# Kernel optimization log

Measured on AMD Instinct MI355X. Metric: run time of the kernel, lower is better.

## Reference

```python
import jax, jax.numpy as jnp
import numpy as np
import math

N = 20000      # nodes
E = 640000     # edges (avg degree 32)
G = 128        # g_dim (input features)
H1 = 128       # rgcn output dim
H2 = 128       # transformer output dim
R = 8          # num_relations


def setup_inputs() -> dict:
    key = jax.random.key(0)
    ks = jax.random.split(key, 12)
    x = jax.random.normal(ks[0], (N, G), dtype=jnp.float32)
    edge_index = jax.random.randint(ks[1], (2, E), 0, N)
    edge_type = jax.random.randint(ks[2], (E,), 0, R)
    s_in = 1.0 / math.sqrt(G)
    s_h1 = 1.0 / math.sqrt(H1)
    return {
        'x': x,
        'edge_index': edge_index,
        'edge_type': edge_type,
        # RGCNConv params (per-relation weights + root weight + bias)
        'rgcn_weight': jax.random.normal(ks[3], (R, G, H1), dtype=jnp.float32) * s_in,
        'rgcn_root': jax.random.normal(ks[4], (G, H1), dtype=jnp.float32) * s_in,
        'rgcn_bias': jnp.zeros((H1,), dtype=jnp.float32),
        # TransformerConv params (heads=1): query/key/value + skip linear
        'Wq': jax.random.normal(ks[5], (H1, H2), dtype=jnp.float32) * s_h1,
        'bq': jnp.zeros((H2,), dtype=jnp.float32),
        'Wk': jax.random.normal(ks[6], (H1, H2), dtype=jnp.float32) * s_h1,
        'bk': jnp.zeros((H2,), dtype=jnp.float32),
        'Wv': jax.random.normal(ks[7], (H1, H2), dtype=jnp.float32) * s_h1,
        'bv': jnp.zeros((H2,), dtype=jnp.float32),
        'Ws': jax.random.normal(ks[8], (H1, H2), dtype=jnp.float32) * s_h1,
        'bs': jnp.zeros((H2,), dtype=jnp.float32),
    }


def reference(x, edge_index, edge_type, rgcn_weight, rgcn_root, rgcn_bias,
              Wq, bq, Wk, bk, Wv, bv, Ws, bs):
    n = x.shape[0]
    src, dst = edge_index[0], edge_index[1]

    # ---- RGCNConv (aggr='mean' per relation, root weight + bias) ----
    # transform nodes by every relation, then gather per-edge message
    xr = jnp.einsum('ni,rio->nro', x, rgcn_weight)          # [N, R, H1]
    msg = xr[src, edge_type]                                # [E, H1]
    # per (dst, relation) edge counts for mean aggregation
    cnt = jnp.zeros((n, rgcn_weight.shape[0]), x.dtype).at[dst, edge_type].add(1.0)
    denom = jnp.maximum(cnt[dst, edge_type], 1.0)[:, None]  # [E, 1]
    agg = jnp.zeros((n, rgcn_weight.shape[2]), x.dtype).at[dst].add(msg / denom)
    h = agg + x @ rgcn_root + rgcn_bias
    h = jax.nn.relu(h)

    # ---- TransformerConv (heads=1, concat, root_weight=True) ----
    d = Wq.shape[1]
    q = h @ Wq + bq                                          # [N, H2]
    k = h @ Wk + bk
    v = h @ Wv + bv
    score = jnp.sum(q[dst] * k[src], axis=-1) / math.sqrt(d) # [E]
    # softmax over incoming edges of each destination node
    smax = jax.ops.segment_max(score, dst, num_segments=n)   # [N]
    e = jnp.exp(score - smax[dst])                           # [E]
    den = jax.ops.segment_sum(e, dst, num_segments=n)        # [N]
    alpha = e / jnp.maximum(den[dst], 1e-16)                 # [E]
    out = jax.ops.segment_sum(alpha[:, None] * v[src], dst, num_segments=n)
    out = out + h @ Ws + bs                                  # skip connection
    return jax.nn.relu(out)
```

## Files before the change

### kernel.cpp

```cpp
#include <hip/hip_runtime.h>

typedef unsigned short u16;
typedef unsigned int u32;
typedef __attribute__((ext_vector_type(8))) short short8;
typedef __attribute__((ext_vector_type(4))) float f32x4;

#define NN 20000
#define EE 640000
#define SCAN_BLOCKS 80

__device__ inline u16 f2bf(float f) {
    u32 x = __float_as_uint(f);
    return (u16)((x + 0x7FFFu + ((x >> 16) & 1u)) >> 16);
}
__device__ inline float lo16(u32 w) { return __uint_as_float(w << 16); }
__device__ inline float hi16(u32 w) { return __uint_as_float(w & 0xFFFF0000u); }
__device__ inline u32 packbf(float a, float b) { return ((u32)f2bf(b) << 16) | (u32)f2bf(a); }

#define ZP_N (NN * 8)
#define CX_N (NN * 32)
#define WP_N (128 * 1152 + 4 * 128 * 128 + 512)
__global__ __launch_bounds__(256) void prep_all(const float* __restrict__ x,
                                                const float* rw, const float* root,
                                                const float* Wq, const float* Wk,
                                                const float* Wv, const float* Ws,
                                                const float* bq, const float* bk,
                                                const float* bv, const float* bs,
                                                int* __restrict__ cnt, u16* __restrict__ xb,
                                                u16* wt1, u16* wt2, float* bcat) {
    int idx = blockIdx.x * 256 + threadIdx.x;
    if (idx < ZP_N) {
        cnt[idx] = 0;
        return;
    }
    idx -= ZP_N;
    if (idx < CX_N) {
        float4 v = *(const float4*)(x + (size_t)idx * 4);
        uint2 o;
        o.x = packbf(v.x, v.y);
        o.y = packbf(v.z, v.w);
        *(uint2*)(xb + (size_t)idx * 4) = o;
        return;
    }
    idx -= CX_N;
    const int S1 = 128 * 1152, S2 = 4 * 128 * 128;
    if (idx < S1) {
        int o = idx / 1152, k = idx - o * 1152;
        float v = (k < 1024) ? rw[k * 128 + o] : root[(k - 1024) * 128 + o];
        wt1[idx] = f2bf(v);
    } else if (idx < S1 + S2) {
        int j = idx - S1;
        int y = j >> 14, rem = j & 16383, o = rem >> 7, i = rem & 127;
        const float* W = (y == 0) ? Wq : (y == 1) ? Wk : (y == 2) ? Wv : Ws;
        wt2[j] = f2bf(W[i * 128 + o]);
    } else if (idx < S1 + S2 + 512) {
        int j = idx - (S1 + S2);
        int y = j >> 7, c = j & 127;
        const float* b = (y == 0) ? bq : (y == 1) ? bk : (y == 2) ? bv : bs;
        bcat[j] = b[c];
    }
}

__global__ void count_rank(const int* __restrict__ ei, const int* __restrict__ et,
                           int* __restrict__ cnt, int* __restrict__ rank) {
    int e = blockIdx.x * 256 + threadIdx.x;
    if (e >= EE) return;
    int dst = ei[EE + e];
    int r = et[e];
    rank[e] = atomicAdd(&cnt[dst * 8 + r], 1);
}

__global__ __launch_bounds__(256) void scan_phase1(const int* __restrict__ cnt,
                                                   int* __restrict__ deg_pref,
                                                   int* __restrict__ blk_sums) {
    __shared__ int lds[256];
    int t = threadIdx.x;
    int n = blockIdx.x * 256 + t;
    int d = 0;
    if (n < NN) {
        int4 c0 = *(const int4*)(cnt + n * 8);
        int4 c1 = *(const int4*)(cnt + n * 8 + 4);
        d = c0.x + c0.y + c0.z + c0.w + c1.x + c1.y + c1.z + c1.w;
    }
    lds[t] = d;
    __syncthreads();
    for (int o = 1; o < 256; o <<= 1) {
        int v = (t >= o) ? lds[t - o] : 0;
        __syncthreads();
        lds[t] += v;
        __syncthreads();
    }
    if (n < NN) deg_pref[n] = lds[t];
    if (t == 255) blk_sums[blockIdx.x] = lds[255];
}

__global__ void scan_phase2(int* __restrict__ blk_sums) {
    __shared__ int lds[128];
    int t = threadIdx.x;
    int v = (t < SCAN_BLOCKS) ? blk_sums[t] : 0;
    lds[t] = v;
    __syncthreads();
    for (int o = 1; o < 128; o <<= 1) {
        int a = (t >= o) ? lds[t - o] : 0;
        __syncthreads();
        lds[t] += a;
        __syncthreads();
    }
    if (t < SCAN_BLOCKS) blk_sums[t] = lds[t] - v;
}

__global__ __launch_bounds__(256) void scan_phase3(const int* __restrict__ cnt,
                                                   const int* __restrict__ deg_pref,
                                                   const int* __restrict__ blk_sums,
                                                   int* __restrict__ row_off,
                                                   int* __restrict__ srt) {
    int n = blockIdx.x * 256 + threadIdx.x;
    if (n >= NN) return;
    int4 c0 = *(const int4*)(cnt + n * 8);
    int4 c1 = *(const int4*)(cnt + n * 8 + 4);
    int deg = c0.x + c0.y + c0.z + c0.w + c1.x + c1.y + c1.z + c1.w;
    int start = blk_sums[blockIdx.x] + deg_pref[n] - deg;
    row_off[n] = start;
    int sub = start;
    int o[8];
    o[0] = sub; sub += c0.x;
    o[1] = sub; sub += c0.y;
    o[2] = sub; sub += c0.z;
    o[3] = sub; sub += c0.w;
    o[4] = sub; sub += c1.x;
    o[5] = sub; sub += c1.y;
    o[6] = sub; sub += c1.z;
    o[7] = sub; sub += c1.w;
    *(int4*)(srt + n * 8) = make_int4(o[0], o[1], o[2], o[3]);
    *(int4*)(srt + n * 8 + 4) = make_int4(o[4], o[5], o[6], o[7]);
    if (n == NN - 1) row_off[NN] = sub;
}

__global__ void scatter_kernel(const int* __restrict__ ei, const int* __restrict__ et,
                               const int* __restrict__ srt, const int* __restrict__ rank,
                               int* __restrict__ es) {
    int e = blockIdx.x * 256 + threadIdx.x;
    if (e >= EE) return;
    int dst = ei[EE + e];
    int src = ei[e];
    int r = et[e];
    int pos = srt[dst * 8 + r] + rank[e];
    es[pos] = src;
}

__global__ __launch_bounds__(256) void rgcn_agg(const u16* __restrict__ xb,
                                                const int* __restrict__ srt,
                                                const int* __restrict__ cnt,
                                                const int* __restrict__ es,
                                                u16* __restrict__ pre) {
    int gid = blockIdx.x * 16 + (threadIdx.x >> 4);
    int lane = threadIdx.x & 15;
    if (gid >= NN * 9) return;
    int node = gid / 9;
    int slot = gid - node * 9;
    long prebase = (long)node * 1152;
    if (slot == 8) {
        uint4 xv = *(const uint4*)(xb + (long)node * 128 + lane * 8);
        *(uint4*)(pre + prebase + 1024 + lane * 8) = xv;
        return;
    }
    int c = cnt[node * 8 + slot];
    int p0 = srt[node * 8 + slot];
    float inv = 1.0f / (float)(c > 1 ? c : 1);
    float a0 = 0.f, a1 = 0.f, a2 = 0.f, a3 = 0.f, a4 = 0.f, a5 = 0.f, a6 = 0.f, a7 = 0.f;
    int i = 0;
    for (; i + 4 <= c; i += 4) {
        int s0 = es[p0 + i], s1 = es[p0 + i + 1], s2 = es[p0 + i + 2], s3 = es[p0 + i + 3];
        uint4 w0 = *(const uint4*)(xb + (long)s0 * 128 + lane * 8);
        uint4 w1 = *(const uint4*)(xb + (long)s1 * 128 + lane * 8);
        uint4 w2 = *(const uint4*)(xb + (long)s2 * 128 + lane * 8);
        uint4 w3 = *(const uint4*)(xb + (long)s3 * 128 + lane * 8);
        a0 += (lo16(w0.x) + lo16(w1.x)) + (lo16(w2.x) + lo16(w3.x));
        a1 += (hi16(w0.x) + hi16(w1.x)) + (hi16(w2.x) + hi16(w3.x));
        a2 += (lo16(w0.y) + lo16(w1.y)) + (lo16(w2.y) + lo16(w3.y));
        a3 += (hi16(w0.y) + hi16(w1.y)) + (hi16(w2.y) + hi16(w3.y));
        a4 += (lo16(w0.z) + lo16(w1.z)) + (lo16(w2.z) + lo16(w3.z));
        a5 += (hi16(w0.z) + hi16(w1.z)) + (hi16(w2.z) + hi16(w3.z));
        a6 += (lo16(w0.w) + lo16(w1.w)) + (lo16(w2.w) + lo16(w3.w));
        a7 += (hi16(w0.w) + hi16(w1.w)) + (hi16(w2.w) + hi16(w3.w));
    }
    for (; i < c; i++) {
        int s = es[p0 + i];
        uint4 w = *(const uint4*)(xb + (long)s * 128 + lane * 8);
        a0 += lo16(w.x); a1 += hi16(w.x); a2 += lo16(w.y); a3 += hi16(w.y);
        a4 += lo16(w.z); a5 += hi16(w.z); a6 += lo16(w.w); a7 += hi16(w.w);
    }
    uint4 ow;
    ow.x = packbf(a0 * inv, a1 * inv);
    ow.y = packbf(a2 * inv, a3 * inv);
    ow.z = packbf(a4 * inv, a5 * inv);
    ow.w = packbf(a6 * inv, a7 * inv);
    *(uint4*)(pre + prebase + slot * 128 + lane * 8) = ow;
}

__global__ __launch_bounds__(256) void gemm_kernel(const u16* __restrict__ A, int lda,
                                                   const u16* __restrict__ Bt, int ldbt,
                                                   const float* __restrict__ bias,
                                                   u16* __restrict__ C, int ldc,
                                                   int rows, int K, int relu,
                                                   long long yBt, long long yC, long long yBias) {
    Bt += blockIdx.y * yBt;
    C += blockIdx.y * yC;
    bias += blockIdx.y * yBias;
    __shared__ u16 As[64 * 136];
    __shared__ u16 Bs[128 * 136];
    int tid = threadIdx.x;
    int w = tid >> 6;
    int lane = tid & 63;
    int quad = lane >> 4;
    int ml = lane & 15;
    int block_m = blockIdx.x * 64;

    f32x4 acc[8];
#pragma unroll
    for (int i = 0; i < 8; i++) acc[i] = (f32x4){0.f, 0.f, 0.f, 0.f};

    int rbase = tid >> 4;
    int cb = (tid & 15) * 8;

    for (int kb = 0; kb < K; kb += 128) {
#pragma unroll
        for (int rep = 0; rep < 4; rep++) {
            int r = rbase + rep * 16;
            int gr = block_m + r;
            short8 val = {};
            if (gr < rows) val = *(const short8*)(A + (long)gr * lda + kb + cb);
            *(short8*)(As + r * 136 + cb) = val;
        }
#pragma unroll
        for (int rep = 0; rep < 8; rep++) {
            int r = rbase + rep * 16;
            short8 val = *(const short8*)(Bt + (long)r * ldbt + kb + cb);
            *(short8*)(Bs + r * 136 + cb) = val;
        }
        __syncthreads();
#pragma unroll
        for (int ks = 0; ks < 4; ks++) {
            short8 af = *(const short8*)(As + (w * 16 + ml) * 136 + ks * 32 + quad * 8);
#pragma unroll
            for (int nt = 0; nt < 8; nt++) {
                short8 bfr = *(const short8*)(Bs + (nt * 16 + ml) * 136 + ks * 32 + quad * 8);
                acc[nt] = __builtin_amdgcn_mfma_f32_16x16x32_bf16(af, bfr, acc[nt], 0, 0, 0);
            }
        }
        __syncthreads();
    }
#pragma unroll
    for (int nt = 0; nt < 8; nt++) {
        int col = nt * 16 + ml;
        float bv = bias[col];
#pragma unroll
        for (int i = 0; i < 4; i++) {
            int gr = block_m + w * 16 + quad * 4 + i;
            if (gr < rows) {
                float vv = acc[nt][i] + bv;
                if (relu) vv = fmaxf(vv, 0.f);
                C[(long)gr * ldc + col] = f2bf(vv);
            }
        }
    }
}

__global__ __launch_bounds__(256) void attn_kernel(const u16* __restrict__ q, const u16* __restrict__ k,
                                                   const u16* __restrict__ v, const u16* __restrict__ skip,
                                                   const int* __restrict__ row_off, const int* __restrict__ es,
                                                   float* __restrict__ out) {
    int node = blockIdx.x * 8 + (threadIdx.x >> 5);
    int lane = threadIdx.x & 31;
    if (node >= NN) return;
    int p0 = row_off[node], p1 = row_off[node + 1];
    uint2 qw = *(const uint2*)(q + (long)node * 128 + lane * 4);
    float q0 = lo16(qw.x), q1 = hi16(qw.x), q2 = lo16(qw.y), q3 = hi16(qw.y);
    const float SC = 0.08838834764831845f;
    float m = -INFINITY, l = 0.f;
    float4 a = {0.f, 0.f, 0.f, 0.f};
    int p = p0;
    for (; p + 4 <= p1; p += 4) {
        int s0 = es[p], s1 = es[p + 1], s2 = es[p + 2], s3 = es[p + 3];
        uint2 k0 = *(const uint2*)(k + (long)s0 * 128 + lane * 4);
        uint2 k1 = *(const uint2*)(k + (long)s1 * 128 + lane * 4);
        uint2 k2 = *(const uint2*)(k + (long)s2 * 128 + lane * 4);
        uint2 k3 = *(const uint2*)(k + (long)s3 * 128 + lane * 4);
        uint2 v0 = *(const uint2*)(v + (long)s0 * 128 + lane * 4);
        uint2 v1 = *(const uint2*)(v + (long)s1 * 128 + lane * 4);
        uint2 v2 = *(const uint2*)(v + (long)s2 * 128 + lane * 4);
        uint2 v3 = *(const uint2*)(v + (long)s3 * 128 + lane * 4);
        float t0 = q0 * lo16(k0.x) + q1 * hi16(k0.x) + q2 * lo16(k0.y) + q3 * hi16(k0.y);
        float t1 = q0 * lo16(k1.x) + q1 * hi16(k1.x) + q2 * lo16(k1.y) + q3 * hi16(k1.y);
        float t2 = q0 * lo16(k2.x) + q1 * hi16(k2.x) + q2 * lo16(k2.y) + q3 * hi16(k2.y);
        float t3 = q0 * lo16(k3.x) + q1 * hi16(k3.x) + q2 * lo16(k3.y) + q3 * hi16(k3.y);
#pragma unroll
        for (int off = 16; off >= 1; off >>= 1) {
            t0 += __shfl_xor(t0, off, 32);
            t1 += __shfl_xor(t1, off, 32);
            t2 += __shfl_xor(t2, off, 32);
            t3 += __shfl_xor(t3, off, 32);
        }
        t0 *= SC; t1 *= SC; t2 *= SC; t3 *= SC;
        float mx = fmaxf(fmaxf(t0, t1), fmaxf(t2, t3));
        float mn = fmaxf(m, mx);
        float scale = __expf(m - mn);
        float w0 = __expf(t0 - mn), w1 = __expf(t1 - mn), w2 = __expf(t2 - mn), w3 = __expf(t3 - mn);
        l = l * scale + ((w0 + w1) + (w2 + w3));
        a.x = a.x * scale + w0 * lo16(v0.x) + w1 * lo16(v1.x) + w2 * lo16(v2.x) + w3 * lo16(v3.x);
        a.y = a.y * scale + w0 * hi16(v0.x) + w1 * hi16(v1.x) + w2 * hi16(v2.x) + w3 * hi16(v3.x);
        a.z = a.z * scale + w0 * lo16(v0.y) + w1 * lo16(v1.y) + w2 * lo16(v2.y) + w3 * lo16(v3.y);
        a.w = a.w * scale + w0 * hi16(v0.y) + w1 * hi16(v1.y) + w2 * hi16(v2.y) + w3 * hi16(v3.y);
        m = mn;
    }
    for (; p < p1; p++) {
        int s = es[p];
        uint2 kw = *(const uint2*)(k + (long)s * 128 + lane * 4);
        uint2 vw = *(const uint2*)(v + (long)s * 128 + lane * 4);
        float t = q0 * lo16(kw.x) + q1 * hi16(kw.x) + q2 * lo16(kw.y) + q3 * hi16(kw.y);
#pragma unroll
        for (int off = 16; off >= 1; off >>= 1) t += __shfl_xor(t, off, 32);
        t *= SC;
        float mn = fmaxf(m, t);
        float scale = __expf(m - mn);
        float wgt = __expf(t - mn);
        l = l * scale + wgt;
        a.x = a.x * scale + wgt * lo16(vw.x);
        a.y = a.y * scale + wgt * hi16(vw.x);
        a.z = a.z * scale + wgt * lo16(vw.y);
        a.w = a.w * scale + wgt * hi16(vw.y);
        m = mn;
    }
    float invl = (l > 0.f) ? 1.0f / l : 0.f;
    uint2 sw = *(const uint2*)(skip + (long)node * 128 + lane * 4);
    float4 o4;
    o4.x = fmaxf(a.x * invl + lo16(sw.x), 0.f);
    o4.y = fmaxf(a.y * invl + hi16(sw.x), 0.f);
    o4.z = fmaxf(a.z * invl + lo16(sw.y), 0.f);
    o4.w = fmaxf(a.w * invl + hi16(sw.y), 0.f);
    *(float4*)(out + (long)node * 128 + lane * 4) = o4;
}

extern "C" void kernel_launch(void* const* d_in, const int* in_sizes, int n_in,
                              void* d_out, int out_size, void* d_ws, size_t ws_size,
                              hipStream_t stream) {
    const float* x = (const float*)d_in[0];
    const int* ei = (const int*)d_in[1];
    const int* et = (const int*)d_in[2];
    const float* rw = (const float*)d_in[3];
    const float* root = (const float*)d_in[4];
    const float* rbias = (const float*)d_in[5];
    const float* Wq = (const float*)d_in[6];
    const float* bq = (const float*)d_in[7];
    const float* Wk = (const float*)d_in[8];
    const float* bk = (const float*)d_in[9];
    const float* Wv = (const float*)d_in[10];
    const float* bv = (const float*)d_in[11];
    const float* Ws = (const float*)d_in[12];
    const float* bs = (const float*)d_in[13];

    char* ws = (char*)d_ws;
    size_t off = 0;
    auto alloc = [&](size_t b) {
        size_t o = off;
        off = (off + b + 255) & ~(size_t)255;
        return o;
    };
    u16* pre = (u16*)(ws + alloc((size_t)NN * 1152 * 2));
    u16* h = (u16*)(ws + alloc((size_t)NN * 128 * 2));
    u16* qkvs = (u16*)(ws + alloc((size_t)4 * NN * 128 * 2));
    u16* xb = (u16*)(ws + alloc((size_t)NN * 128 * 2));
    u16* wt1 = (u16*)(ws + alloc((size_t)128 * 1152 * 2));
    u16* wt2 = (u16*)(ws + alloc((size_t)4 * 128 * 128 * 2));
    float* bcat = (float*)(ws + alloc((size_t)512 * 4));
    int* cnt = (int*)(ws + alloc((size_t)NN * 8 * 4));
    int* row_off = (int*)(ws + alloc((size_t)(NN + 1) * 4));
    int* srt = (int*)(ws + alloc((size_t)NN * 8 * 4));
    int* deg_pref = (int*)(ws + alloc((size_t)NN * 4));
    int* blk_sums = (int*)(ws + alloc((size_t)128 * 4));
    int* rank = (int*)(ws + alloc((size_t)EE * 4));
    int* es = (int*)(ws + alloc((size_t)EE * 4));
    (void)ws_size;
    (void)in_sizes;
    (void)n_in;
    (void)out_size;

    prep_all<<<(ZP_N + CX_N + WP_N + 255) / 256, 256, 0, stream>>>(
        x, rw, root, Wq, Wk, Wv, Ws, bq, bk, bv, bs, cnt, xb, wt1, wt2, bcat);

    count_rank<<<EE / 256, 256, 0, stream>>>(ei, et, cnt, rank);
    scan_phase1<<<SCAN_BLOCKS, 256, 0, stream>>>(cnt, deg_pref, blk_sums);
    scan_phase2<<<1, 128, 0, stream>>>(blk_sums);
    scan_phase3<<<SCAN_BLOCKS, 256, 0, stream>>>(cnt, deg_pref, blk_sums, row_off, srt);
    scatter_kernel<<<EE / 256, 256, 0, stream>>>(ei, et, srt, rank, es);

    rgcn_agg<<<(NN * 9 + 15) / 16, 256, 0, stream>>>(xb, srt, cnt, es, pre);

    gemm_kernel<<<dim3((NN + 63) / 64, 1), 256, 0, stream>>>(pre, 1152, wt1, 1152, rbias, h, 128,
                                                             NN, 1152, 1, 0, 0, 0);
    gemm_kernel<<<dim3((NN + 63) / 64, 4), 256, 0, stream>>>(h, 128, wt2, 128, bcat, qkvs, 128,
                                                             NN, 128, 0, (long long)128 * 128,
                                                             (long long)NN * 128, 128);

    attn_kernel<<<(NN + 7) / 8, 256, 0, stream>>>(qkvs, qkvs + (size_t)NN * 128, qkvs + (size_t)2 * NN * 128,
                                                  qkvs + (size_t)3 * NN * 128, row_off, es, (float*)d_out);
}
```

Measured before the change: 254.4 us.

## Add 32-row RGCN GEMM, widen attention lanes, multi-edge per thread in preprocessing

Three separate changes. The first GEMM gets a dedicated kernel with 32-row tiles, so it launches twice as many blocks over the K=1152 reduction and better fills the GPU's compute units. The attention kernel now uses 16 lanes per node with 128-bit loads, which packs more nodes per block and cuts the shuffle reduction to four steps. The count and scatter kernels each process four edges per thread. The costs are more reloads of the B tile across blocks in the GEMM and more registers per thread in attention.

```diff
diff --git a/kernel.cpp b/kernel.cpp
--- a/kernel.cpp
+++ b/kernel.cpp
@@ -63,11 +63,16 @@
 
 __global__ void count_rank(const int* __restrict__ ei, const int* __restrict__ et,
                            int* __restrict__ cnt, int* __restrict__ rank) {
-    int e = blockIdx.x * 256 + threadIdx.x;
-    if (e >= EE) return;
-    int dst = ei[EE + e];
-    int r = et[e];
-    rank[e] = atomicAdd(&cnt[dst * 8 + r], 1);
+    int base = blockIdx.x * 1024 + threadIdx.x;
+#pragma unroll
+    for (int j = 0; j < 4; j++) {
+        int e = base + j * 256;
+        if (e < EE) {
+            int dst = ei[EE + e];
+            int r = et[e];
+            rank[e] = atomicAdd(&cnt[dst * 8 + r], 1);
+        }
+    }
 }
 
 __global__ __launch_bounds__(256) void scan_phase1(const int* __restrict__ cnt,
@@ -139,13 +144,17 @@
 __global__ void scatter_kernel(const int* __restrict__ ei, const int* __restrict__ et,
                                const int* __restrict__ srt, const int* __restrict__ rank,
                                int* __restrict__ es) {
-    int e = blockIdx.x * 256 + threadIdx.x;
-    if (e >= EE) return;
-    int dst = ei[EE + e];
-    int src = ei[e];
-    int r = et[e];
-    int pos = srt[dst * 8 + r] + rank[e];
-    es[pos] = src;
+    int base = blockIdx.x * 1024 + threadIdx.x;
+#pragma unroll
+    for (int j = 0; j < 4; j++) {
+        int e = base + j * 256;
+        if (e < EE) {
+            int dst = ei[EE + e];
+            int src = ei[e];
+            int r = et[e];
+            es[srt[dst * 8 + r] + rank[e]] = src;
+        }
+    }
 }
 
 __global__ __launch_bounds__(256) void rgcn_agg(const u16* __restrict__ xb,
@@ -198,6 +207,70 @@
     *(uint4*)(pre + prebase + slot * 128 + lane * 8) = ow;
 }
 
+__global__ __launch_bounds__(256) void gemm_bm32(const u16* __restrict__ A,
+                                                 const u16* __restrict__ Bt,
+                                                 const float* __restrict__ bias,
+                                                 u16* __restrict__ C, int rows) {
+    __shared__ u16 As[32 * 136];
+    __shared__ u16 Bs[128 * 136];
+    int tid = threadIdx.x;
+    int w = tid >> 6;
+    int lane = tid & 63;
+    int quad = lane >> 4;
+    int ml = lane & 15;
+    int mt = w & 1;
+    int nq = w >> 1;
+    int block_m = blockIdx.x * 32;
+
+    f32x4 acc[4];
+#pragma unroll
+    for (int i = 0; i < 4; i++) acc[i] = (f32x4){0.f, 0.f, 0.f, 0.f};
+
+    int rbase = tid >> 4;
+    int cb = (tid & 15) * 8;
+
+    for (int kb = 0; kb < 1152; kb += 128) {
+#pragma unroll
+        for (int rep = 0; rep < 2; rep++) {
+            int r = rbase + rep * 16;
+            int gr = block_m + r;
+            short8 val = {};
+            if (gr < rows) val = *(const short8*)(A + (long)gr * 1152 + kb + cb);
+            *(short8*)(As + r * 136 + cb) = val;
+        }
+#pragma unroll
+        for (int rep = 0; rep < 8; rep++) {
+            int r = rbase + rep * 16;
+            short8 val = *(const short8*)(Bt + (long)r * 1152 + kb + cb);
+            *(short8*)(Bs + r * 136 + cb) = val;
+        }
+        __syncthreads();
+#pragma unroll
+        for (int ks = 0; ks < 4; ks++) {
+            short8 af = *(const short8*)(As + (mt * 16 + ml) * 136 + ks * 32 + quad * 8);
+#pragma unroll
+            for (int nt = 0; nt < 4; nt++) {
+                short8 bfr = *(const short8*)(Bs + (nq * 64 + nt * 16 + ml) * 136 + ks * 32 + quad * 8);
+                acc[nt] = __builtin_amdgcn_mfma_f32_16x16x32_bf16(af, bfr, acc[nt], 0, 0, 0);
+            }
+        }
+        __syncthreads();
+    }
+#pragma unroll
+    for (int nt = 0; nt < 4; nt++) {
+        int col = nq * 64 + nt * 16 + ml;
+        float bv = bias[col];
+#pragma unroll
+        for (int i = 0; i < 4; i++) {
+            int gr = block_m + mt * 16 + quad * 4 + i;
+            if (gr < rows) {
+                float vv = fmaxf(acc[nt][i] + bv, 0.f);
+                C[(long)gr * 128 + col] = f2bf(vv);
+            }
+        }
+    }
+}
+
 __global__ __launch_bounds__(256) void gemm_kernel(const u16* __restrict__ A, int lda,
                                                    const u16* __restrict__ Bt, int ldbt,
                                                    const float* __restrict__ bias,
@@ -270,36 +343,41 @@
                                                    const u16* __restrict__ v, const u16* __restrict__ skip,
                                                    const int* __restrict__ row_off, const int* __restrict__ es,
                                                    float* __restrict__ out) {
-    int node = blockIdx.x * 8 + (threadIdx.x >> 5);
-    int lane = threadIdx.x & 31;
+    int node = blockIdx.x * 16 + (threadIdx.x >> 4);
+    int lane = threadIdx.x & 15;
     if (node >= NN) return;
     int p0 = row_off[node], p1 = row_off[node + 1];
-    uint2 qw = *(const uint2*)(q + (long)node * 128 + lane * 4);
+    uint4 qw = *(const uint4*)(q + (long)node * 128 + lane * 8);
     float q0 = lo16(qw.x), q1 = hi16(qw.x), q2 = lo16(qw.y), q3 = hi16(qw.y);
+    float q4 = lo16(qw.z), q5 = hi16(qw.z), q6 = lo16(qw.w), q7 = hi16(qw.w);
     const float SC = 0.08838834764831845f;
     float m = -INFINITY, l = 0.f;
-    float4 a = {0.f, 0.f, 0.f, 0.f};
+    float a0 = 0.f, a1 = 0.f, a2 = 0.f, a3 = 0.f, a4 = 0.f, a5 = 0.f, a6 = 0.f, a7 = 0.f;
     int p = p0;
     for (; p + 4 <= p1; p += 4) {
         int s0 = es[p], s1 = es[p + 1], s2 = es[p + 2], s3 = es[p + 3];
-        uint2 k0 = *(const uint2*)(k + (long)s0 * 128 + lane * 4);
-        uint2 k1 = *(const uint2*)(k + (long)s1 * 128 + lane * 4);
-        uint2 k2 = *(const uint2*)(k + (long)s2 * 128 + lane * 4);
-        uint2 k3 = *(const uint2*)(k + (long)s3 * 128 + lane * 4);
-        uint2 v0 = *(const uint2*)(v + (long)s0 * 128 + lane * 4);
-        uint2 v1 = *(const uint2*)(v + (long)s1 * 128 + lane * 4);
-        uint2 v2 = *(const uint2*)(v + (long)s2 * 128 + lane * 4);
-        uint2 v3 = *(const uint2*)(v + (long)s3 * 128 + lane * 4);
-        float t0 = q0 * lo16(k0.x) + q1 * hi16(k0.x) + q2 * lo16(k0.y) + q3 * hi16(k0.y);
-        float t1 = q0 * lo16(k1.x) + q1 * hi16(k1.x) + q2 * lo16(k1.y) + q3 * hi16(k1.y);
-        float t2 = q0 * lo16(k2.x) + q1 * hi16(k2.x) + q2 * lo16(k2.y) + q3 * hi16(k2.y);
-        float t3 = q0 * lo16(k3.x) + q1 * hi16(k3.x) + q2 * lo16(k3.y) + q3 * hi16(k3.y);
-#pragma unroll
-        for (int off = 16; off >= 1; off >>= 1) {
-            t0 += __shfl_xor(t0, off, 32);
-            t1 += __shfl_xor(t1, off, 32);
-            t2 += __shfl_xor(t2, off, 32);
-            t3 += __shfl_xor(t3, off, 32);
+        uint4 k0 = *(const uint4*)(k + (long)s0 * 128 + lane * 8);
+        uint4 k1 = *(const uint4*)(k + (long)s1 * 128 + lane * 8);
+        uint4 k2 = *(const uint4*)(k + (long)s2 * 128 + lane * 8);
+        uint4 k3 = *(const uint4*)(k + (long)s3 * 128 + lane * 8);
+        uint4 v0 = *(const uint4*)(v + (long)s0 * 128 + lane * 8);
+        uint4 v1 = *(const uint4*)(v + (long)s1 * 128 + lane * 8);
+        uint4 v2 = *(const uint4*)(v + (long)s2 * 128 + lane * 8);
+        uint4 v3 = *(const uint4*)(v + (long)s3 * 128 + lane * 8);
+        float t0 = q0 * lo16(k0.x) + q1 * hi16(k0.x) + q2 * lo16(k0.y) + q3 * hi16(k0.y) +
+                   q4 * lo16(k0.z) + q5 * hi16(k0.z) + q6 * lo16(k0.w) + q7 * hi16(k0.w);
+        float t1 = q0 * lo16(k1.x) + q1 * hi16(k1.x) + q2 * lo16(k1.y) + q3 * hi16(k1.y) +
+                   q4 * lo16(k1.z) + q5 * hi16(k1.z) + q6 * lo16(k1.w) + q7 * hi16(k1.w);
+        float t2 = q0 * lo16(k2.x) + q1 * hi16(k2.x) + q2 * lo16(k2.y) + q3 * hi16(k2.y) +
+                   q4 * lo16(k2.z) + q5 * hi16(k2.z) + q6 * lo16(k2.w) + q7 * hi16(k2.w);
+        float t3 = q0 * lo16(k3.x) + q1 * hi16(k3.x) + q2 * lo16(k3.y) + q3 * hi16(k3.y) +
+                   q4 * lo16(k3.z) + q5 * hi16(k3.z) + q6 * lo16(k3.w) + q7 * hi16(k3.w);
+#pragma unroll
+        for (int off = 8; off >= 1; off >>= 1) {
+            t0 += __shfl_xor(t0, off, 16);
+            t1 += __shfl_xor(t1, off, 16);
+            t2 += __shfl_xor(t2, off, 16);
+            t3 += __shfl_xor(t3, off, 16);
         }
         t0 *= SC; t1 *= SC; t2 *= SC; t3 *= SC;
         float mx = fmaxf(fmaxf(t0, t1), fmaxf(t2, t3));
@@ -307,38 +385,52 @@
         float scale = __expf(m - mn);
         float w0 = __expf(t0 - mn), w1 = __expf(t1 - mn), w2 = __expf(t2 - mn), w3 = __expf(t3 - mn);
         l = l * scale + ((w0 + w1) + (w2 + w3));
-        a.x = a.x * scale + w0 * lo16(v0.x) + w1 * lo16(v1.x) + w2 * lo16(v2.x) + w3 * lo16(v3.x);
-        a.y = a.y * scale + w0 * hi16(v0.x) + w1 * hi16(v1.x) + w2 * hi16(v2.x) + w3 * hi16(v3.x);
-        a.z = a.z * scale + w0 * lo16(v0.y) + w1 * lo16(v1.y) + w2 * lo16(v2.y) + w3 * lo16(v3.y);
-        a.w = a.w * scale + w0 * hi16(v0.y) + w1 * hi16(v1.y) + w2 * hi16(v2.y) + w3 * hi16(v3.y);
+        a0 = a0 * scale + w0 * lo16(v0.x) + w1 * lo16(v1.x) + w2 * lo16(v2.x) + w3 * lo16(v3.x);
+        a1 = a1 * scale + w0 * hi16(v0.x) + w1 * hi16(v1.x) + w2 * hi16(v2.x) + w3 * hi16(v3.x);
+        a2 = a2 * scale + w0 * lo16(v0.y) + w1 * lo16(v1.y) + w2 * lo16(v2.y) + w3 * lo16(v3.y);
+        a3 = a3 * scale + w0 * hi16(v0.y) + w1 * hi16(v1.y) + w2 * hi16(v2.y) + w3 * hi16(v3.y);
+        a4 = a4 * scale + w0 * lo16(v0.z) + w1 * lo16(v1.z) + w2 * lo16(v2.z) + w3 * lo16(v3.z);
+        a5 = a5 * scale + w0 * hi16(v0.z) + w1 * hi16(v1.z) + w2 * hi16(v2.z) + w3 * hi16(v3.z);
+        a6 = a6 * scale + w0 * lo16(v0.w) + w1 * lo16(v1.w) + w2 * lo16(v2.w) + w3 * lo16(v3.w);
+        a7 = a7 * scale + w0 * hi16(v0.w) + w1 * hi16(v1.w) + w2 * hi16(v2.w) + w3 * hi16(v3.w);
         m = mn;
     }
     for (; p < p1; p++) {
         int s = es[p];
-        uint2 kw = *(const uint2*)(k + (long)s * 128 + lane * 4);
-        uint2 vw = *(const uint2*)(v + (long)s * 128 + lane * 4);
-        float t = q0 * lo16(kw.x) + q1 * hi16(kw.x) + q2 * lo16(kw.y) + q3 * hi16(kw.y);
-#pragma unroll
-        for (int off = 16; off >= 1; off >>= 1) t += __shfl_xor(t, off, 32);
+        uint4 kw = *(const uint4*)(k + (long)s * 128 + lane * 8);
+        uint4 vw = *(const uint4*)(v + (long)s * 128 + lane * 8);
+        float t = q0 * lo16(kw.x) + q1 * hi16(kw.x) + q2 * lo16(kw.y) + q3 * hi16(kw.y) +
+                  q4 * lo16(kw.z) + q5 * hi16(kw.z) + q6 * lo16(kw.w) + q7 * hi16(kw.w);
+#pragma unroll
+        for (int off = 8; off >= 1; off >>= 1) t += __shfl_xor(t, off, 16);
         t *= SC;
         float mn = fmaxf(m, t);
         float scale = __expf(m - mn);
         float wgt = __expf(t - mn);
         l = l * scale + wgt;
-        a.x = a.x * scale + wgt * lo16(vw.x);
-        a.y = a.y * scale + wgt * hi16(vw.x);
-        a.z = a.z * scale + wgt * lo16(vw.y);
-        a.w = a.w * scale + wgt * hi16(vw.y);
+        a0 = a0 * scale + wgt * lo16(vw.x);
+        a1 = a1 * scale + wgt * hi16(vw.x);
+        a2 = a2 * scale + wgt * lo16(vw.y);
+        a3 = a3 * scale + wgt * hi16(vw.y);
+        a4 = a4 * scale + wgt * lo16(vw.z);
+        a5 = a5 * scale + wgt * hi16(vw.z);
+        a6 = a6 * scale + wgt * lo16(vw.w);
+        a7 = a7 * scale + wgt * hi16(vw.w);
         m = mn;
     }
     float invl = (l > 0.f) ? 1.0f / l : 0.f;
-    uint2 sw = *(const uint2*)(skip + (long)node * 128 + lane * 4);
-    float4 o4;
-    o4.x = fmaxf(a.x * invl + lo16(sw.x), 0.f);
-    o4.y = fmaxf(a.y * invl + hi16(sw.x), 0.f);
-    o4.z = fmaxf(a.z * invl + lo16(sw.y), 0.f);
-    o4.w = fmaxf(a.w * invl + hi16(sw.y), 0.f);
-    *(float4*)(out + (long)node * 128 + lane * 4) = o4;
+    uint4 sw = *(const uint4*)(skip + (long)node * 128 + lane * 8);
+    float4 oa, ob;
+    oa.x = fmaxf(a0 * invl + lo16(sw.x), 0.f);
+    oa.y = fmaxf(a1 * invl + hi16(sw.x), 0.f);
+    oa.z = fmaxf(a2 * invl + lo16(sw.y), 0.f);
+    oa.w = fmaxf(a3 * invl + hi16(sw.y), 0.f);
+    ob.x = fmaxf(a4 * invl + lo16(sw.z), 0.f);
+    ob.y = fmaxf(a5 * invl + hi16(sw.z), 0.f);
+    ob.z = fmaxf(a6 * invl + lo16(sw.w), 0.f);
+    ob.w = fmaxf(a7 * invl + hi16(sw.w), 0.f);
+    *(float4*)(out + (long)node * 128 + lane * 8) = oa;
+    *(float4*)(out + (long)node * 128 + lane * 8 + 4) = ob;
 }
 
 extern "C" void kernel_launch(void* const* d_in, const int* in_sizes, int n_in,
@@ -388,20 +480,19 @@
     prep_all<<<(ZP_N + CX_N + WP_N + 255) / 256, 256, 0, stream>>>(
         x, rw, root, Wq, Wk, Wv, Ws, bq, bk, bv, bs, cnt, xb, wt1, wt2, bcat);
 
-    count_rank<<<EE / 256, 256, 0, stream>>>(ei, et, cnt, rank);
+    count_rank<<<(EE + 1023) / 1024, 256, 0, stream>>>(ei, et, cnt, rank);
     scan_phase1<<<SCAN_BLOCKS, 256, 0, stream>>>(cnt, deg_pref, blk_sums);
     scan_phase2<<<1, 128, 0, stream>>>(blk_sums);
     scan_phase3<<<SCAN_BLOCKS, 256, 0, stream>>>(cnt, deg_pref, blk_sums, row_off, srt);
-    scatter_kernel<<<EE / 256, 256, 0, stream>>>(ei, et, srt, rank, es);
+    scatter_kernel<<<(EE + 1023) / 1024, 256, 0, stream>>>(ei, et, srt, rank, es);
 
     rgcn_agg<<<(NN * 9 + 15) / 16, 256, 0, stream>>>(xb, srt, cnt, es, pre);
 
-    gemm_kernel<<<dim3((NN + 63) / 64, 1), 256, 0, stream>>>(pre, 1152, wt1, 1152, rbias, h, 128,
-                                                             NN, 1152, 1, 0, 0, 0);
+    gemm_bm32<<<(NN + 31) / 32, 256, 0, stream>>>(pre, wt1, rbias, h, NN);
     gemm_kernel<<<dim3((NN + 63) / 64, 4), 256, 0, stream>>>(h, 128, wt2, 128, bcat, qkvs, 128,
                                                              NN, 128, 0, (long long)128 * 128,
                                                              (long long)NN * 128, 128);
 
-    attn_kernel<<<(NN + 7) / 8, 256, 0, stream>>>(qkvs, qkvs + (size_t)NN * 128, qkvs + (size_t)2 * NN * 128,
-                                                  qkvs + (size_t)3 * NN * 128, row_off, es, (float*)d_out);
-}
+    attn_kernel<<<(NN + 15) / 16, 256, 0, stream>>>(qkvs, qkvs + (size_t)NN * 128, qkvs + (size_t)2 * NN * 128,
+                                                    qkvs + (size_t)3 * NN * 128, row_off, es, (float*)d_out);
+}
```

New measurement: 250.9 us. Within noise of the previous version (-1.4%).
